# Performance work log

Measured on AMD Instinct MI355X. Metric: run time of the kernel, lower is better.

The kernel has to match this reference:

```python
import jax, jax.numpy as jnp
import numpy as np

B_GRAPHS = 64
N_PER = 8192
N = B_GRAPHS * N_PER          # 524288 nodes
E = N * 24                    # 12582912 edges
F0 = 8                        # num_node_features
FE = 4                        # num_edge_features
HID = 5                       # embedding_size, heads=1
ACT = 4                       # num_actions
GOAL = 6                      # goal_size
EPS = 1e-5


def _graph_norm(x, batch, w, b, ms):
    # PyG GraphNorm: per-graph mean/var with learnable mean_scale
    cnt = jax.ops.segment_sum(jnp.ones((x.shape[0],), x.dtype), batch, num_segments=B_GRAPHS)[:, None]
    mean = jax.ops.segment_sum(x, batch, num_segments=B_GRAPHS) / cnt
    sub = x - ms * mean[batch]
    var = jax.ops.segment_sum(sub * sub, batch, num_segments=B_GRAPHS) / cnt
    return w * sub * jax.lax.rsqrt(var[batch] + EPS) + b


def _gatv2(x, edge_index, edge_attr, Wl, bl, Wr, br, We, att, bo):
    # GATv2Conv, heads=1, add_self_loops=True (self-loop edge_attr = mean of edge_attr)
    n = x.shape[0]
    loop = jnp.arange(n, dtype=edge_index.dtype)
    src = jnp.concatenate([edge_index[0], loop])
    dst = jnp.concatenate([edge_index[1], loop])
    ea = jnp.concatenate([edge_attr, jnp.broadcast_to(edge_attr.mean(0), (n, edge_attr.shape[1]))], axis=0)
    xl = x @ Wl + bl            # source transform [n, HID]
    xr = x @ Wr + br            # target transform [n, HID]
    xl_src = xl[src]            # [E+n, HID]
    e = jax.nn.leaky_relu(xl_src + xr[dst] + ea @ We, 0.2)
    logits = e @ att            # [E+n]
    m = jax.ops.segment_max(logits, dst, num_segments=n)
    ex = jnp.exp(logits - m[dst])
    alpha = ex / jax.ops.segment_sum(ex, dst, num_segments=n)[dst]
    return jax.ops.segment_sum(alpha[:, None] * xl_src, dst, num_segments=n) + bo


def reference(x, edge_index, edge_attr, batch, current_node_ids, action_mask, one_hot_goal,
              gn_w, gn_b, gn_ms,
              Wl1, bl1, Wr1, br1, We1, att1, bo1,
              Wl2, bl2, Wr2, br2, We2, att2, bo2,
              Wv1, bv1, Wv2, bv2, Wa1, ba1, Wa2, ba2):
    x = _graph_norm(x, batch, gn_w, gn_b, gn_ms)
    identity = x
    h = jax.nn.relu(_gatv2(x, edge_index, edge_attr, Wl1, bl1, Wr1, br1, We1, att1, bo1))
    x = jnp.concatenate([h, identity], axis=1)    # [N, 13]
    identity = x
    h = jax.nn.relu(_gatv2(x, edge_index, edge_attr, Wl2, bl2, Wr2, br2, We2, att2, bo2))
    x = jnp.concatenate([h, identity], axis=1)    # [N, 18]
    cnt = jnp.bincount(batch, length=B_GRAPHS)
    pool = jax.ops.segment_sum(x, batch, num_segments=B_GRAPHS) / cnt[:, None].astype(x.dtype)
    offsets = jnp.concatenate([jnp.zeros((1,), cnt.dtype), jnp.cumsum(cnt)[:-1]])
    xg = x[current_node_ids + offsets]            # [B, 18]
    feat = jnp.concatenate([xg, pool, one_hot_goal], axis=1)  # [B, 42]
    adv = jax.nn.relu(feat @ Wa1 + ba1) @ Wa2 + ba2
    val = jax.nn.relu(feat @ Wv1 + bv1) @ Wv2 + bv2
    q = val + adv - adv.mean(axis=1, keepdims=True)
    return jnp.where(action_mask == 0, jnp.asarray(-1e8, q.dtype), q)


def setup_inputs():
    key = jax.random.key(0)
    k = jax.random.split(key, 24)
    lin_w = lambda kk, i, o: (jax.random.normal(kk, (i, o), jnp.float32) / np.sqrt(i)).astype(jnp.float32)
    x = jax.random.normal(k[0], (N, F0), jnp.float32)
    g = jax.random.randint(k[1], (E,), 0, B_GRAPHS)
    src = g * N_PER + jax.random.randint(k[2], (E,), 0, N_PER)
    dst = g * N_PER + jax.random.randint(k[3], (E,), 0, N_PER)
    edge_index = jnp.stack([src, dst]).astype(jnp.int32)
    edge_attr = jax.random.normal(k[4], (E, FE), jnp.float32)
    batch = (jnp.arange(N) // N_PER).astype(jnp.int32)
    current_node_ids = jax.random.randint(k[5], (B_GRAPHS,), 0, N_PER).astype(jnp.int32)
    action_mask = jax.random.randint(k[6], (B_GRAPHS, ACT), 0, 2).astype(jnp.int32)
    one_hot_goal = jax.nn.one_hot(jax.random.randint(k[7], (B_GRAPHS,), 0, GOAL), GOAL, dtype=jnp.float32)
    inp = dict(x=x, edge_index=edge_index, edge_attr=edge_attr, batch=batch,
               current_node_ids=current_node_ids, action_mask=action_mask, one_hot_goal=one_hot_goal)
    inp.update(gn_w=jnp.ones((F0,)), gn_b=jnp.zeros((F0,)), gn_ms=jnp.ones((F0,)))
    inp.update(Wl1=lin_w(k[8], F0, HID), bl1=jnp.zeros((HID,)), Wr1=lin_w(k[9], F0, HID), br1=jnp.zeros((HID,)),
               We1=lin_w(k[10], FE, HID), att1=jax.random.normal(k[11], (HID,), jnp.float32), bo1=jnp.zeros((HID,)))
    inp.update(Wl2=lin_w(k[12], 13, HID), bl2=jnp.zeros((HID,)), Wr2=lin_w(k[13], 13, HID), br2=jnp.zeros((HID,)),
               We2=lin_w(k[14], FE, HID), att2=jax.random.normal(k[15], (HID,), jnp.float32), bo2=jnp.zeros((HID,)))
    inp.update(Wv1=lin_w(k[16], 42, 10), bv1=jnp.zeros((10,)), Wv2=lin_w(k[17], 10, 1), bv2=jnp.zeros((1,)),
               Wa1=lin_w(k[18], 42, 10), ba1=jnp.zeros((10,)), Wa2=lin_w(k[19], 10, ACT), ba2=jnp.zeros((ACT,)))
    return inp
```

## Files before the change

kernel.cpp:

```cpp
#include <hip/hip_runtime.h>
#include <hip/hip_bf16.h>
#include <stdint.h>

#define NG   64
#define NPER 8192
#define NN   (NG * NPER)
#define NE   (NN * 24)
#define F0   8

#define NBIN   1024
#define BROWS  512
#define BCAP   13312
#define SCHUNK 8192
#define NBLK   (NE / SCHUNK)

__device__ __forceinline__ void atomAddF(float* p, float v) {
    unsafeAtomicAdd(p, v);
}

__device__ __forceinline__ uint32_t pk_bf16(float a, float b) {
    return (__float_as_uint(a) >> 16) | (__float_as_uint(b) & 0xFFFF0000u);
}
__device__ __forceinline__ float lo_bf16(uint32_t u) { return __uint_as_float(u << 16); }
__device__ __forceinline__ float hi_bf16(uint32_t u) { return __uint_as_float(u & 0xFFFF0000u); }

__global__ void k_stats(const float* __restrict__ x, float* __restrict__ stats) {
    int b = blockIdx.x;
    int g = b >> 2;
    int seg = b & 3;
    int t = threadIdx.x;
    float sum[8] = {0,0,0,0,0,0,0,0};
    float sq[8]  = {0,0,0,0,0,0,0,0};
    int base = g * NPER + seg * 2048;
    for (int r = t; r < 2048; r += 256) {
        const float* row = x + (size_t)(base + r) * F0;
        #pragma unroll
        for (int f = 0; f < 8; f++) { float v = row[f]; sum[f] += v; sq[f] += v * v; }
    }
    #pragma unroll
    for (int f = 0; f < 8; f++) {
        float s = sum[f], q = sq[f];
        for (int off = 32; off > 0; off >>= 1) {
            s += __shfl_down(s, off);
            q += __shfl_down(q, off);
        }
        if ((t & 63) == 0) {
            atomAddF(stats + g*16 + f, s);
            atomAddF(stats + g*16 + 8 + f, q);
        }
    }
}

__global__ void k_norm(const float* __restrict__ x, const float* __restrict__ stats,
                       const float* __restrict__ gw, const float* __restrict__ gb,
                       const float* __restrict__ gms,
                       const float* __restrict__ Wl, const float* __restrict__ bl,
                       const float* __restrict__ Wr, const float* __restrict__ br,
                       float* __restrict__ xn, uint4* __restrict__ xlc,
                       float* __restrict__ xr1) {
    int g = blockIdx.x >> 5;
    int n = blockIdx.x * 256 + threadIdx.x;
    const float invc = 1.0f / (float)NPER;
    float xnf[8];
    const float* row = x + (size_t)n * F0;
    #pragma unroll
    for (int f = 0; f < 8; f++) {
        float m   = stats[g*16 + f] * invc;
        float ex2 = stats[g*16 + 8 + f] * invc;
        float ms  = gms[f];
        float var = ex2 - 2.0f*ms*m*m + ms*ms*m*m;
        float sub = row[f] - ms * m;
        xnf[f] = gw[f] * sub * rsqrtf(var + 1e-5f) + gb[f];
    }
    float* xnr = xn + (size_t)n * 8;
    #pragma unroll
    for (int f = 0; f < 8; f++) xnr[f] = xnf[f];
    float xlv[5], xrv[5];
    #pragma unroll
    for (int j = 0; j < 5; j++) {
        float a = bl[j], b = br[j];
        #pragma unroll
        for (int f = 0; f < 8; f++) { a += xnf[f] * Wl[f*5 + j]; b += xnf[f] * Wr[f*5 + j]; }
        xlv[j] = a; xrv[j] = b;
    }
    uint4 p;
    p.x = pk_bf16(xlv[0], xlv[1]);
    p.y = pk_bf16(xlv[2], xlv[3]);
    p.z = pk_bf16(xlv[4], 0.0f);
    p.w = 0u;
    xlc[n] = p;
    float* xrr = xr1 + (size_t)n * 8;
    #pragma unroll
    for (int j = 0; j < 5; j++) xrr[j] = xrv[j];
    #pragma unroll
    for (int j = 5; j < 8; j++) xrr[j] = 0.0f;
}

__global__ __launch_bounds__(1024) void k_bin(
        const int* __restrict__ src, const int* __restrict__ dst,
        const float4* __restrict__ eattr,
        unsigned* __restrict__ gfill, uint2* __restrict__ payload,
        float* __restrict__ easum) {
    __shared__ unsigned lc[NBIN];
    __shared__ unsigned lstart[NBIN];
    __shared__ unsigned lalloc[NBIN];
    __shared__ unsigned lbase[NBIN];
    __shared__ uint2 stage[SCHUNK];
    __shared__ float ls[16][4];
    int t = threadIdx.x;
    int base = blockIdx.x * SCHUNK;
    lc[t] = 0u;
    __syncthreads();
    int dc[SCHUNK/1024];
    #pragma unroll
    for (int k = 0; k < SCHUNK/1024; k++) dc[k] = dst[base + k*1024 + t];
    #pragma unroll
    for (int k = 0; k < SCHUNK/1024; k++)
        atomicAdd(&lc[((unsigned)dc[k]) >> 9], 1u);
    __syncthreads();
    lstart[t] = lc[t];
    __syncthreads();
    for (int off = 1; off < NBIN; off <<= 1) {
        unsigned u = (t >= off) ? lstart[t - off] : 0u;
        __syncthreads();
        lstart[t] += u;
        __syncthreads();
    }
    unsigned excl = lstart[t] - lc[t];
    __syncthreads();
    lstart[t] = excl;
    lalloc[t] = excl;
    lbase[t]  = lc[t] ? atomicAdd(&gfill[t], lc[t]) : 0u;
    __syncthreads();
    float e0 = 0.f, e1 = 0.f, e2 = 0.f, e3 = 0.f;
    #pragma unroll
    for (int k = 0; k < SCHUNK/1024; k++) {
        int e = base + k*1024 + t;
        int s = src[e];
        int d = dc[k];
        float4 ea = eattr[e];
        e0 += ea.x; e1 += ea.y; e2 += ea.z; e3 += ea.w;
        unsigned b = ((unsigned)d) >> 9;
        uint32_t xw = (unsigned)(s & 8191) | ((unsigned)(d & 511) << 13) | (b << 22);
        uint32_t yw = __builtin_amdgcn_cvt_pk_fp8_f32(ea.z, ea.w,
                        __builtin_amdgcn_cvt_pk_fp8_f32(ea.x, ea.y, 0, false), true);
        unsigned pos = atomicAdd(&lalloc[b], 1u);
        stage[pos] = make_uint2(xw, yw);
    }
    __syncthreads();
    for (int i = t; i < SCHUNK; i += 1024) {
        uint2 r = stage[i];
        unsigned b = r.x >> 22;
        unsigned loc = lbase[b] + ((unsigned)i - lstart[b]);
        if (loc < BCAP) payload[(size_t)b * BCAP + loc] = r;
    }
    for (int off = 32; off > 0; off >>= 1) {
        e0 += __shfl_down(e0, off); e1 += __shfl_down(e1, off);
        e2 += __shfl_down(e2, off); e3 += __shfl_down(e3, off);
    }
    int wv = t >> 6;
    if ((t & 63) == 0) { ls[wv][0]=e0; ls[wv][1]=e1; ls[wv][2]=e2; ls[wv][3]=e3; }
    __syncthreads();
    if (t < 4) {
        float v = 0.f;
        #pragma unroll
        for (int k = 0; k < 16; k++) v += ls[k][t];
        atomAddF(easum + t, v);
    }
}

template<int PASS>
__global__ __launch_bounds__(1024) void k_edge(
        const uint2* __restrict__ payload, const unsigned* __restrict__ gfill,
        const uint4* __restrict__ xlcv, const float* __restrict__ xrf,
        const float* __restrict__ xn, const float* __restrict__ h1in,
        const float* __restrict__ We, const float* __restrict__ att,
        const float* __restrict__ bo, const float* __restrict__ easum,
        const float* __restrict__ Wl2, const float* __restrict__ bl2,
        const float* __restrict__ Wr2, const float* __restrict__ br2,
        float* __restrict__ h1out, uint4* __restrict__ xl2c, float* __restrict__ xr2,
        const int* __restrict__ cur, float* __restrict__ pool, float* __restrict__ xg) {
    __shared__ uint2 stage[BCAP + 2];
    __shared__ unsigned cnt_s[BROWS];
    __shared__ unsigned scan_s[BROWS];
    __shared__ unsigned alloc_s[BROWS];
    __shared__ float lsum[16][18];
    int t = threadIdx.x;
    int bin = ((blockIdx.x & 7) << 7) + (blockIdx.x >> 3);
    int g = bin >> 4;

    unsigned CNT = gfill[bin];
    if (CNT > BCAP) CNT = BCAP;
    const uint2* pA = payload + (size_t)bin * BCAP;

    uint2 rcv[13];
    #pragma unroll
    for (int k = 0; k < 13; ++k) {
        unsigned idx = (unsigned)(k * 1024) + (unsigned)t;
        rcv[k] = (idx < CNT) ? pA[idx] : make_uint2(0u, 0u);
    }
    if (t < BROWS) cnt_s[t] = 0u;
    __syncthreads();
    #pragma unroll
    for (int k = 0; k < 13; ++k) {
        unsigned idx = (unsigned)(k * 1024) + (unsigned)t;
        if (idx < CNT) atomicAdd(&cnt_s[(rcv[k].x >> 13) & 511u], 1u);
    }
    __syncthreads();
    if (t < BROWS) scan_s[t] = cnt_s[t];
    __syncthreads();
    for (int off = 1; off < BROWS; off <<= 1) {
        unsigned u = 0;
        if (t < BROWS && t >= off) u = scan_s[t - off];
        __syncthreads();
        if (t < BROWS) scan_s[t] += u;
        __syncthreads();
    }
    if (t < BROWS) alloc_s[t] = scan_s[t] - cnt_s[t];
    __syncthreads();
    #pragma unroll
    for (int k = 0; k < 13; ++k) {
        unsigned idx = (unsigned)(k * 1024) + (unsigned)t;
        if (idx < CNT) {
            unsigned pos = atomicAdd(&alloc_s[(rcv[k].x >> 13) & 511u], 1u);
            stage[pos] = rcv[k];
        }
    }
    __syncthreads();

    int r = t >> 1, sub = t & 1;
    int n = (bin << 9) + r;
    unsigned end   = scan_s[r];
    unsigned start = end - cnt_s[r];

    float w0[5], w1[5], w2[5], w3[5], av[5];
    #pragma unroll
    for (int j = 0; j < 5; j++) {
        w0[j] = We[j]; w1[j] = We[5+j]; w2[j] = We[10+j]; w3[j] = We[15+j];
        av[j] = att[j];
    }
    const uint4* xlg = xlcv + ((size_t)g << 13);
    const float4* xr4 = (const float4*)(xrf + (size_t)n * 8);
    float4 q0 = xr4[0], q1 = xr4[1];
    float xrv[5] = {q0.x, q0.y, q0.z, q0.w, q1.x};

    float acc[5] = {0.f, 0.f, 0.f, 0.f, 0.f};
    float aw = 0.f;

    unsigned i0 = start + (unsigned)sub;
    uint2 rcur = stage[i0];
    uint4 xcur = xlg[rcur.x & 8191u];
    for (unsigned i = i0; i < end; i += 2) {
        uint2 rnext = stage[i + 2];
        uint4 xnext = xlg[rnext.x & 8191u];
        float xs[5] = {lo_bf16(xcur.x), hi_bf16(xcur.x),
                       lo_bf16(xcur.y), hi_bf16(xcur.y), lo_bf16(xcur.z)};
        float eax = __builtin_amdgcn_cvt_f32_fp8(rcur.y, 0);
        float eay = __builtin_amdgcn_cvt_f32_fp8(rcur.y, 1);
        float eaz = __builtin_amdgcn_cvt_f32_fp8(rcur.y, 2);
        float eaw = __builtin_amdgcn_cvt_f32_fp8(rcur.y, 3);
        float lg = 0.f;
        #pragma unroll
        for (int j = 0; j < 5; j++) {
            float z = xs[j] + xrv[j] + w0[j]*eax + w1[j]*eay + w2[j]*eaz + w3[j]*eaw;
            z = z > 0.f ? z : 0.2f * z;
            lg += z * av[j];
        }
        float w = __expf(lg);
        aw += w;
        #pragma unroll
        for (int j = 0; j < 5; j++) acc[j] += w * xs[j];
        rcur = rnext; xcur = xnext;
    }
    aw += __shfl_xor(aw, 1);
    #pragma unroll
    for (int j = 0; j < 5; j++) acc[j] += __shfl_xor(acc[j], 1);

    const float invE = 1.0f / (float)NE;
    float eaM[5];
    #pragma unroll
    for (int j = 0; j < 5; j++)
        eaM[j] = (easum[0]*w0[j] + easum[1]*w1[j] + easum[2]*w2[j] + easum[3]*w3[j]) * invE;
    uint4 xw = xlcv[n];
    float xlv[5] = {lo_bf16(xw.x), hi_bf16(xw.x),
                    lo_bf16(xw.y), hi_bf16(xw.y), lo_bf16(xw.z)};
    float lg = 0.f;
    #pragma unroll
    for (int j = 0; j < 5; j++) {
        float z = xlv[j] + xrv[j] + eaM[j];
        z = z > 0.f ? z : 0.2f * z;
        lg += z * av[j];
    }
    float wsl = __expf(lg);
    float den = aw + wsl;
    float h[5];
    #pragma unroll
    for (int j = 0; j < 5; j++) {
        float v = (acc[j] + wsl * xlv[j]) / den + bo[j];
        h[j] = v > 0.f ? v : 0.f;
    }
    const float4* xnr = (const float4*)(xn + (size_t)n * 8);
    float4 xa = xnr[0], xb = xnr[1];

    if (PASS == 1) {
        if (!sub) {
            float x2[13];
            #pragma unroll
            for (int j = 0; j < 5; j++) x2[j] = h[j];
            x2[5] = xa.x; x2[6] = xa.y; x2[7] = xa.z; x2[8] = xa.w;
            x2[9] = xb.x; x2[10] = xb.y; x2[11] = xb.z; x2[12] = xb.w;
            float4* h1r = (float4*)(h1out + (size_t)n * 8);
            h1r[0] = make_float4(h[0], h[1], h[2], h[3]);
            (h1out + (size_t)n * 8)[4] = h[4];
            float l2[5], r2[5];
            #pragma unroll
            for (int j = 0; j < 5; j++) {
                float a = bl2[j], b = br2[j];
                #pragma unroll
                for (int k = 0; k < 13; k++) { a += x2[k] * Wl2[k*5 + j]; b += x2[k] * Wr2[k*5 + j]; }
                l2[j] = a; r2[j] = b;
            }
            uint4 p;
            p.x = pk_bf16(l2[0], l2[1]);
            p.y = pk_bf16(l2[2], l2[3]);
            p.z = pk_bf16(l2[4], 0.0f);
            p.w = 0u;
            xl2c[n] = p;
            float4* xr2r = (float4*)(xr2 + (size_t)n * 8);
            xr2r[0] = make_float4(r2[0], r2[1], r2[2], r2[3]);
            xr2r[1] = make_float4(r2[4], 0.f, 0.f, 0.f);
        }
    } else {
        float x3[18];
        #pragma unroll
        for (int j = 0; j < 5; j++) x3[j] = h[j];
        const float* h1r = h1in + (size_t)n * 8;
        #pragma unroll
        for (int j = 0; j < 5; j++) x3[5 + j] = h1r[j];
        x3[10] = xa.x; x3[11] = xa.y; x3[12] = xa.z; x3[13] = xa.w;
        x3[14] = xb.x; x3[15] = xb.y; x3[16] = xb.z; x3[17] = xb.w;
        int wv = t >> 6;
        #pragma unroll
        for (int f = 0; f < 18; f++) {
            float v = sub ? 0.f : x3[f];
            for (int off = 32; off > 0; off >>= 1) v += __shfl_down(v, off);
            if ((t & 63) == 0) lsum[wv][f] = v;
        }
        __syncthreads();
        if (t < 18) {
            float v = 0.f;
            #pragma unroll
            for (int k = 0; k < 16; k++) v += lsum[k][t];
            atomAddF(pool + g*18 + t, v);
        }
        if (!sub && ((n & (NPER - 1)) == cur[g])) {
            #pragma unroll
            for (int f = 0; f < 18; f++) xg[g*18 + f] = x3[f];
        }
    }
}

__global__ void k_head(const float* __restrict__ xg, const float* __restrict__ pool,
                       const float* __restrict__ goal, const int* __restrict__ am,
                       const float* __restrict__ Wv1, const float* __restrict__ bv1,
                       const float* __restrict__ Wv2, const float* __restrict__ bv2,
                       const float* __restrict__ Wa1, const float* __restrict__ ba1,
                       const float* __restrict__ Wa2, const float* __restrict__ ba2,
                       float* __restrict__ out) {
    int g = threadIdx.x;
    if (g >= NG) return;
    float feat[42];
    #pragma unroll
    for (int f = 0; f < 18; f++) feat[f] = xg[g*18 + f];
    #pragma unroll
    for (int f = 0; f < 18; f++) feat[18 + f] = pool[g*18 + f] * (1.0f / (float)NPER);
    #pragma unroll
    for (int f = 0; f < 6; f++) feat[36 + f] = goal[g*6 + f];
    float hv[10], ha[10];
    #pragma unroll
    for (int j = 0; j < 10; j++) {
        float a = bv1[j], b = ba1[j];
        for (int k = 0; k < 42; k++) { a += feat[k] * Wv1[k*10 + j]; b += feat[k] * Wa1[k*10 + j]; }
        hv[j] = a > 0.f ? a : 0.f;
        ha[j] = b > 0.f ? b : 0.f;
    }
    float val = bv2[0];
    #pragma unroll
    for (int k = 0; k < 10; k++) val += hv[k] * Wv2[k];
    float adv[4];
    #pragma unroll
    for (int a2 = 0; a2 < 4; a2++) {
        float s = ba2[a2];
        #pragma unroll
        for (int k = 0; k < 10; k++) s += ha[k] * Wa2[k*4 + a2];
        adv[a2] = s;
    }
    float mean = 0.25f * (adv[0] + adv[1] + adv[2] + adv[3]);
    #pragma unroll
    for (int a2 = 0; a2 < 4; a2++) {
        float q = val + adv[a2] - mean;
        if (am[g*4 + a2] == 0) q = -1e8f;
        out[g*4 + a2] = q;
    }
}

extern "C" void kernel_launch(void* const* d_in, const int* in_sizes, int n_in,
                              void* d_out, int out_size, void* d_ws, size_t ws_size,
                              hipStream_t stream) {
    const float* x     = (const float*)d_in[0];
    const int*   ei    = (const int*)  d_in[1];
    const float* eattr = (const float*)d_in[2];
    const int*   cur   = (const int*)  d_in[4];
    const int*   am    = (const int*)  d_in[5];
    const float* goal  = (const float*)d_in[6];
    const float* gw    = (const float*)d_in[7];
    const float* gb    = (const float*)d_in[8];
    const float* gms   = (const float*)d_in[9];
    const float* Wl1   = (const float*)d_in[10];
    const float* bl1   = (const float*)d_in[11];
    const float* Wr1   = (const float*)d_in[12];
    const float* br1   = (const float*)d_in[13];
    const float* We1   = (const float*)d_in[14];
    const float* att1  = (const float*)d_in[15];
    const float* bo1   = (const float*)d_in[16];
    const float* Wl2   = (const float*)d_in[17];
    const float* bl2   = (const float*)d_in[18];
    const float* Wr2   = (const float*)d_in[19];
    const float* br2   = (const float*)d_in[20];
    const float* We2   = (const float*)d_in[21];
    const float* att2  = (const float*)d_in[22];
    const float* bo2   = (const float*)d_in[23];
    const float* Wv1   = (const float*)d_in[24];
    const float* bv1   = (const float*)d_in[25];
    const float* Wv2   = (const float*)d_in[26];
    const float* bv2   = (const float*)d_in[27];
    const float* Wa1   = (const float*)d_in[28];
    const float* ba1   = (const float*)d_in[29];
    const float* Wa2   = (const float*)d_in[30];
    const float* ba2   = (const float*)d_in[31];

    float* ws   = (float*)d_ws;
    float* xn   = ws;
    float* xr1  = xn  + (size_t)NN * 8;
    float* xr2  = xr1 + (size_t)NN * 8;
    float* h1   = xr2 + (size_t)NN * 8;
    uint4* xlc  = (uint4*)(h1 + (size_t)NN * 8);
    uint4* xl2c = xlc + (size_t)NN;
    uint2* payload = (uint2*)(xl2c + (size_t)NN);
    unsigned* gfill = (unsigned*)(payload + (size_t)NBIN * BCAP + 4);
    float* stats = (float*)(gfill + NBIN);
    float* easum = stats + NG * 16;
    float* pool  = easum + 4;
    float* xg    = pool + NG * 18;

    size_t zbytes = (size_t)(NBIN + NG*16 + 4 + NG*18) * 4;
    hipMemsetAsync(gfill, 0, zbytes, stream);

    k_stats<<<256, 256, 0, stream>>>(x, stats);
    k_norm<<<NN/256, 256, 0, stream>>>(x, stats, gw, gb, gms, Wl1, bl1, Wr1, br1,
                                       xn, xlc, xr1);
    k_bin<<<NBLK, 1024, 0, stream>>>(ei, ei + NE, (const float4*)eattr,
                                     gfill, payload, easum);
    k_edge<1><<<NBIN, 1024, 0, stream>>>(payload, gfill, xlc, xr1, xn, nullptr,
                                         We1, att1, bo1, easum,
                                         Wl2, bl2, Wr2, br2,
                                         h1, xl2c, xr2,
                                         nullptr, nullptr, nullptr);
    k_edge<2><<<NBIN, 1024, 0, stream>>>(payload, gfill, xl2c, xr2, xn, h1,
                                         We2, att2, bo2, easum,
                                         nullptr, nullptr, nullptr, nullptr,
                                         nullptr, nullptr, nullptr,
                                         cur, pool, xg);
    k_head<<<1, 64, 0, stream>>>(xg, pool, goal, am, Wv1, bv1, Wv2, bv2,
                                 Wa1, ba1, Wa2, ba2, (float*)d_out);
}
```

Baseline: 686.6 us.

## Use wave-shuffle scans, vectorized row IO, batched LDS atomics, deeper gather prefetch

Replaces the barrier-heavy Hillis-Steele shared-memory scans in the binning and edge kernels with wave-level shuffle scans plus a small cross-wave pass, cutting the number of __syncthreads. It vectorizes the per-node row loads and stores in the stats and norm kernels to float4, and batches the LDS atomics ahead of the stage writes. The edge loop now prefetches two iterations ahead instead of one, which needs more stage padding and workspace offset. The layer-2 linear transform is also split so the two sub-lanes each compute one of Wl2/Wr2, removing idle lanes.

```diff
diff --git a/kernel.cpp b/kernel.cpp
--- a/kernel.cpp
+++ b/kernel.cpp
@@ -33,9 +33,13 @@
     float sq[8]  = {0,0,0,0,0,0,0,0};
     int base = g * NPER + seg * 2048;
     for (int r = t; r < 2048; r += 256) {
-        const float* row = x + (size_t)(base + r) * F0;
-        #pragma unroll
-        for (int f = 0; f < 8; f++) { float v = row[f]; sum[f] += v; sq[f] += v * v; }
+        const float4* row = (const float4*)(x + (size_t)(base + r) * F0);
+        float4 ra = row[0], rb = row[1];
+        float v0=ra.x,v1=ra.y,v2=ra.z,v3=ra.w,v4=rb.x,v5=rb.y,v6=rb.z,v7=rb.w;
+        sum[0]+=v0; sq[0]+=v0*v0; sum[1]+=v1; sq[1]+=v1*v1;
+        sum[2]+=v2; sq[2]+=v2*v2; sum[3]+=v3; sq[3]+=v3*v3;
+        sum[4]+=v4; sq[4]+=v4*v4; sum[5]+=v5; sq[5]+=v5*v5;
+        sum[6]+=v6; sq[6]+=v6*v6; sum[7]+=v7; sq[7]+=v7*v7;
     }
     #pragma unroll
     for (int f = 0; f < 8; f++) {
@@ -62,19 +66,21 @@
     int n = blockIdx.x * 256 + threadIdx.x;
     const float invc = 1.0f / (float)NPER;
     float xnf[8];
-    const float* row = x + (size_t)n * F0;
+    const float4* row4 = (const float4*)(x + (size_t)n * F0);
+    float4 ra = row4[0], rb = row4[1];
+    float rv[8] = {ra.x, ra.y, ra.z, ra.w, rb.x, rb.y, rb.z, rb.w};
     #pragma unroll
     for (int f = 0; f < 8; f++) {
         float m   = stats[g*16 + f] * invc;
         float ex2 = stats[g*16 + 8 + f] * invc;
         float ms  = gms[f];
         float var = ex2 - 2.0f*ms*m*m + ms*ms*m*m;
-        float sub = row[f] - ms * m;
+        float sub = rv[f] - ms * m;
         xnf[f] = gw[f] * sub * rsqrtf(var + 1e-5f) + gb[f];
     }
-    float* xnr = xn + (size_t)n * 8;
-    #pragma unroll
-    for (int f = 0; f < 8; f++) xnr[f] = xnf[f];
+    float4* xnr = (float4*)(xn + (size_t)n * 8);
+    xnr[0] = make_float4(xnf[0], xnf[1], xnf[2], xnf[3]);
+    xnr[1] = make_float4(xnf[4], xnf[5], xnf[6], xnf[7]);
     float xlv[5], xrv[5];
     #pragma unroll
     for (int j = 0; j < 5; j++) {
@@ -89,11 +95,9 @@
     p.z = pk_bf16(xlv[4], 0.0f);
     p.w = 0u;
     xlc[n] = p;
-    float* xrr = xr1 + (size_t)n * 8;
-    #pragma unroll
-    for (int j = 0; j < 5; j++) xrr[j] = xrv[j];
-    #pragma unroll
-    for (int j = 5; j < 8; j++) xrr[j] = 0.0f;
+    float4* xrr = (float4*)(xr1 + (size_t)n * 8);
+    xrr[0] = make_float4(xrv[0], xrv[1], xrv[2], xrv[3]);
+    xrr[1] = make_float4(xrv[4], 0.f, 0.f, 0.f);
 }
 
 __global__ __launch_bounds__(1024) void k_bin(
@@ -107,7 +111,9 @@
     __shared__ unsigned lbase[NBIN];
     __shared__ uint2 stage[SCHUNK];
     __shared__ float ls[16][4];
+    __shared__ unsigned wsum[16];
     int t = threadIdx.x;
+    int lane = t & 63, wv = t >> 6;
     int base = blockIdx.x * SCHUNK;
     lc[t] = 0u;
     __syncthreads();
@@ -118,35 +124,48 @@
     for (int k = 0; k < SCHUNK/1024; k++)
         atomicAdd(&lc[((unsigned)dc[k]) >> 9], 1u);
     __syncthreads();
-    lstart[t] = lc[t];
-    __syncthreads();
-    for (int off = 1; off < NBIN; off <<= 1) {
-        unsigned u = (t >= off) ? lstart[t - off] : 0u;
-        __syncthreads();
-        lstart[t] += u;
-        __syncthreads();
-    }
-    unsigned excl = lstart[t] - lc[t];
-    __syncthreads();
+    unsigned c = lc[t];
+    unsigned s = c;
+    #pragma unroll
+    for (int d = 1; d < 64; d <<= 1) {
+        unsigned u = (unsigned)__shfl_up((int)s, d);
+        if (lane >= d) s += u;
+    }
+    if (lane == 63) wsum[wv] = s;
+    __syncthreads();
+    if (t < 16) {
+        unsigned v = wsum[t], sv = v;
+        #pragma unroll
+        for (int d = 1; d < 16; d <<= 1) {
+            unsigned u = (unsigned)__shfl_up((int)sv, d);
+            if (t >= d) sv += u;
+        }
+        wsum[t] = sv - v;
+    }
+    __syncthreads();
+    unsigned excl = s + wsum[wv] - c;
     lstart[t] = excl;
     lalloc[t] = excl;
-    lbase[t]  = lc[t] ? atomicAdd(&gfill[t], lc[t]) : 0u;
+    lbase[t]  = c ? atomicAdd(&gfill[t], c) : 0u;
     __syncthreads();
     float e0 = 0.f, e1 = 0.f, e2 = 0.f, e3 = 0.f;
+    unsigned xwv[SCHUNK/1024], ywv[SCHUNK/1024], bv[SCHUNK/1024], pos[SCHUNK/1024];
     #pragma unroll
     for (int k = 0; k < SCHUNK/1024; k++) {
         int e = base + k*1024 + t;
-        int s = src[e];
+        int sv2 = src[e];
         int d = dc[k];
         float4 ea = eattr[e];
         e0 += ea.x; e1 += ea.y; e2 += ea.z; e3 += ea.w;
-        unsigned b = ((unsigned)d) >> 9;
-        uint32_t xw = (unsigned)(s & 8191) | ((unsigned)(d & 511) << 13) | (b << 22);
-        uint32_t yw = __builtin_amdgcn_cvt_pk_fp8_f32(ea.z, ea.w,
-                        __builtin_amdgcn_cvt_pk_fp8_f32(ea.x, ea.y, 0, false), true);
-        unsigned pos = atomicAdd(&lalloc[b], 1u);
-        stage[pos] = make_uint2(xw, yw);
-    }
+        bv[k] = ((unsigned)d) >> 9;
+        xwv[k] = (unsigned)(sv2 & 8191) | ((unsigned)(d & 511) << 13) | (bv[k] << 22);
+        ywv[k] = __builtin_amdgcn_cvt_pk_fp8_f32(ea.z, ea.w,
+                    __builtin_amdgcn_cvt_pk_fp8_f32(ea.x, ea.y, 0, false), true);
+    }
+    #pragma unroll
+    for (int k = 0; k < SCHUNK/1024; k++) pos[k] = atomicAdd(&lalloc[bv[k]], 1u);
+    #pragma unroll
+    for (int k = 0; k < SCHUNK/1024; k++) stage[pos[k]] = make_uint2(xwv[k], ywv[k]);
     __syncthreads();
     for (int i = t; i < SCHUNK; i += 1024) {
         uint2 r = stage[i];
@@ -158,7 +177,6 @@
         e0 += __shfl_down(e0, off); e1 += __shfl_down(e1, off);
         e2 += __shfl_down(e2, off); e3 += __shfl_down(e3, off);
     }
-    int wv = t >> 6;
     if ((t & 63) == 0) { ls[wv][0]=e0; ls[wv][1]=e1; ls[wv][2]=e2; ls[wv][3]=e3; }
     __syncthreads();
     if (t < 4) {
@@ -180,12 +198,14 @@
         const float* __restrict__ Wr2, const float* __restrict__ br2,
         float* __restrict__ h1out, uint4* __restrict__ xl2c, float* __restrict__ xr2,
         const int* __restrict__ cur, float* __restrict__ pool, float* __restrict__ xg) {
-    __shared__ uint2 stage[BCAP + 2];
+    __shared__ uint2 stage[BCAP + 6];
     __shared__ unsigned cnt_s[BROWS];
     __shared__ unsigned scan_s[BROWS];
     __shared__ unsigned alloc_s[BROWS];
+    __shared__ unsigned wscan[8];
     __shared__ float lsum[16][18];
     int t = threadIdx.x;
+    int lane = t & 63, wvi = t >> 6;
     int bin = ((blockIdx.x & 7) << 7) + (blockIdx.x >> 3);
     int g = bin >> 4;
 
@@ -207,24 +227,44 @@
         if (idx < CNT) atomicAdd(&cnt_s[(rcv[k].x >> 13) & 511u], 1u);
     }
     __syncthreads();
-    if (t < BROWS) scan_s[t] = cnt_s[t];
-    __syncthreads();
-    for (int off = 1; off < BROWS; off <<= 1) {
-        unsigned u = 0;
-        if (t < BROWS && t >= off) u = scan_s[t - off];
-        __syncthreads();
-        if (t < BROWS) scan_s[t] += u;
-        __syncthreads();
-    }
-    if (t < BROWS) alloc_s[t] = scan_s[t] - cnt_s[t];
-    __syncthreads();
+    unsigned c = 0, s = 0;
+    if (t < BROWS) {
+        c = cnt_s[t];
+        s = c;
+        #pragma unroll
+        for (int d = 1; d < 64; d <<= 1) {
+            unsigned u = (unsigned)__shfl_up((int)s, d);
+            if (lane >= d) s += u;
+        }
+        if (lane == 63) wscan[wvi] = s;
+    }
+    __syncthreads();
+    if (t < 8) {
+        unsigned v = wscan[t], sv = v;
+        #pragma unroll
+        for (int d = 1; d < 8; d <<= 1) {
+            unsigned u = (unsigned)__shfl_up((int)sv, d);
+            if (t >= d) sv += u;
+        }
+        wscan[t] = sv - v;
+    }
+    __syncthreads();
+    if (t < BROWS) {
+        unsigned incl = s + wscan[wvi];
+        scan_s[t]  = incl;
+        alloc_s[t] = incl - c;
+    }
+    __syncthreads();
+    unsigned pos[13];
     #pragma unroll
     for (int k = 0; k < 13; ++k) {
         unsigned idx = (unsigned)(k * 1024) + (unsigned)t;
-        if (idx < CNT) {
-            unsigned pos = atomicAdd(&alloc_s[(rcv[k].x >> 13) & 511u], 1u);
-            stage[pos] = rcv[k];
-        }
+        pos[k] = (idx < CNT) ? atomicAdd(&alloc_s[(rcv[k].x >> 13) & 511u], 1u) : 0u;
+    }
+    #pragma unroll
+    for (int k = 0; k < 13; ++k) {
+        unsigned idx = (unsigned)(k * 1024) + (unsigned)t;
+        if (idx < CNT) stage[pos[k]] = rcv[k];
     }
     __syncthreads();
 
@@ -248,17 +288,19 @@
     float aw = 0.f;
 
     unsigned i0 = start + (unsigned)sub;
-    uint2 rcur = stage[i0];
-    uint4 xcur = xlg[rcur.x & 8191u];
+    uint2 r0 = stage[i0];
+    uint4 x0 = xlg[r0.x & 8191u];
+    uint2 r1 = stage[i0 + 2];
+    uint4 x1 = xlg[r1.x & 8191u];
     for (unsigned i = i0; i < end; i += 2) {
-        uint2 rnext = stage[i + 2];
-        uint4 xnext = xlg[rnext.x & 8191u];
-        float xs[5] = {lo_bf16(xcur.x), hi_bf16(xcur.x),
-                       lo_bf16(xcur.y), hi_bf16(xcur.y), lo_bf16(xcur.z)};
-        float eax = __builtin_amdgcn_cvt_f32_fp8(rcur.y, 0);
-        float eay = __builtin_amdgcn_cvt_f32_fp8(rcur.y, 1);
-        float eaz = __builtin_amdgcn_cvt_f32_fp8(rcur.y, 2);
-        float eaw = __builtin_amdgcn_cvt_f32_fp8(rcur.y, 3);
+        uint2 rn = stage[i + 4];
+        uint4 xf = xlg[rn.x & 8191u];
+        float xs[5] = {lo_bf16(x0.x), hi_bf16(x0.x),
+                       lo_bf16(x0.y), hi_bf16(x0.y), lo_bf16(x0.z)};
+        float eax = __builtin_amdgcn_cvt_f32_fp8(r0.y, 0);
+        float eay = __builtin_amdgcn_cvt_f32_fp8(r0.y, 1);
+        float eaz = __builtin_amdgcn_cvt_f32_fp8(r0.y, 2);
+        float eaw = __builtin_amdgcn_cvt_f32_fp8(r0.y, 3);
         float lg = 0.f;
         #pragma unroll
         for (int j = 0; j < 5; j++) {
@@ -270,7 +312,7 @@
         aw += w;
         #pragma unroll
         for (int j = 0; j < 5; j++) acc[j] += w * xs[j];
-        rcur = rnext; xcur = xnext;
+        r0 = r1; x0 = x1; r1 = rn; x1 = xf;
     }
     aw += __shfl_xor(aw, 1);
     #pragma unroll
@@ -303,32 +345,35 @@
     float4 xa = xnr[0], xb = xnr[1];
 
     if (PASS == 1) {
-        if (!sub) {
-            float x2[13];
+        float x2[13];
+        #pragma unroll
+        for (int j = 0; j < 5; j++) x2[j] = h[j];
+        x2[5] = xa.x; x2[6] = xa.y; x2[7] = xa.z; x2[8] = xa.w;
+        x2[9] = xb.x; x2[10] = xb.y; x2[11] = xb.z; x2[12] = xb.w;
+        const float* Wx = sub ? Wr2 : Wl2;
+        const float* bx = sub ? br2 : bl2;
+        float o[5];
+        #pragma unroll
+        for (int j = 0; j < 5; j++) {
+            float a = bx[j];
             #pragma unroll
-            for (int j = 0; j < 5; j++) x2[j] = h[j];
-            x2[5] = xa.x; x2[6] = xa.y; x2[7] = xa.z; x2[8] = xa.w;
-            x2[9] = xb.x; x2[10] = xb.y; x2[11] = xb.z; x2[12] = xb.w;
+            for (int k = 0; k < 13; k++) a += x2[k] * Wx[k*5 + j];
+            o[j] = a;
+        }
+        if (sub) {
+            float4* xr2r = (float4*)(xr2 + (size_t)n * 8);
+            xr2r[0] = make_float4(o[0], o[1], o[2], o[3]);
+            xr2r[1] = make_float4(o[4], 0.f, 0.f, 0.f);
             float4* h1r = (float4*)(h1out + (size_t)n * 8);
             h1r[0] = make_float4(h[0], h[1], h[2], h[3]);
             (h1out + (size_t)n * 8)[4] = h[4];
-            float l2[5], r2[5];
-            #pragma unroll
-            for (int j = 0; j < 5; j++) {
-                float a = bl2[j], b = br2[j];
-                #pragma unroll
-                for (int k = 0; k < 13; k++) { a += x2[k] * Wl2[k*5 + j]; b += x2[k] * Wr2[k*5 + j]; }
-                l2[j] = a; r2[j] = b;
-            }
+        } else {
             uint4 p;
-            p.x = pk_bf16(l2[0], l2[1]);
-            p.y = pk_bf16(l2[2], l2[3]);
-            p.z = pk_bf16(l2[4], 0.0f);
+            p.x = pk_bf16(o[0], o[1]);
+            p.y = pk_bf16(o[2], o[3]);
+            p.z = pk_bf16(o[4], 0.0f);
             p.w = 0u;
             xl2c[n] = p;
-            float4* xr2r = (float4*)(xr2 + (size_t)n * 8);
-            xr2r[0] = make_float4(r2[0], r2[1], r2[2], r2[3]);
-            xr2r[1] = make_float4(r2[4], 0.f, 0.f, 0.f);
         }
     } else {
         float x3[18];
@@ -339,12 +384,11 @@
         for (int j = 0; j < 5; j++) x3[5 + j] = h1r[j];
         x3[10] = xa.x; x3[11] = xa.y; x3[12] = xa.z; x3[13] = xa.w;
         x3[14] = xb.x; x3[15] = xb.y; x3[16] = xb.z; x3[17] = xb.w;
-        int wv = t >> 6;
         #pragma unroll
         for (int f = 0; f < 18; f++) {
             float v = sub ? 0.f : x3[f];
             for (int off = 32; off > 0; off >>= 1) v += __shfl_down(v, off);
-            if ((t & 63) == 0) lsum[wv][f] = v;
+            if ((t & 63) == 0) lsum[wvi][f] = v;
         }
         __syncthreads();
         if (t < 18) {
@@ -447,7 +491,7 @@
     uint4* xlc  = (uint4*)(h1 + (size_t)NN * 8);
     uint4* xl2c = xlc + (size_t)NN;
     uint2* payload = (uint2*)(xl2c + (size_t)NN);
-    unsigned* gfill = (unsigned*)(payload + (size_t)NBIN * BCAP + 4);
+    unsigned* gfill = (unsigned*)(payload + (size_t)NBIN * BCAP + 8);
     float* stats = (float*)(gfill + NBIN);
     float* easum = stats + NG * 16;
     float* pool  = easum + 4;
```

Measured after the change: 681.2 us. Within noise of the previous version (-0.8%).
